# Performance work log

Measured on AMD Instinct MI355X. Metric: run time of the kernel, lower is better.

The kernel has to match this reference:

```python
import jax, jax.numpy as jnp
import numpy as np

B, Q, K, D = 32, 1024, 1024, 128

def setup_inputs() -> dict:
    key = jax.random.key(0)
    kq, kk, kv, kl = jax.random.split(key, 4)
    return {
        "queries": jax.random.normal(kq, (B, Q, D), dtype=jnp.float32),
        "keys": jax.random.normal(kk, (B, K, D), dtype=jnp.float32),
        "values": jax.random.normal(kv, (B, K, D), dtype=jnp.float32),
        "valid_length": jax.random.randint(kl, (B,), 1, K + 1),
    }

def reference(queries, keys, values, valid_length):
    d = queries.shape[-1]
    # scores: [B, Q, K]
    scores = jnp.einsum("bqd,bkd->bqk", queries, keys) / jnp.sqrt(jnp.float32(d))
    # length mask: position k is valid iff k < valid_length[b]
    mask = jnp.arange(keys.shape[1])[None, None, :] < valid_length[:, None, None]
    scores = jnp.where(mask, scores, jnp.float32(-1e9))
    attn = jax.nn.softmax(scores, axis=-1)
    # dropout module is identity in eval / p=0
    return jnp.einsum("bqk,bkv->bqv", attn, values)
```

## Files before the change

### kernel.cpp

```cpp
#include <hip/hip_runtime.h>
#include <hip/hip_bf16.h>
#include <stdint.h>

#define B_    32
#define QLEN  1024
#define KSEQ  1024
#define DIM   128
#define NKT   (KSEQ / 64)
#define SCALE 0.08838834764831845f

typedef __attribute__((ext_vector_type(8))) short  short8;
typedef __attribute__((ext_vector_type(4))) float  floatx4;
typedef unsigned int u32;

__device__ __forceinline__ u32 f2bf(float x) {
  union { float f; u32 u; } v; v.f = x;
  return (v.u + 0x7FFF + ((v.u >> 16) & 1)) >> 16;
}
__device__ __forceinline__ u32 pack2(float lo, float hi) {
  return f2bf(lo) | (f2bf(hi) << 16);
}

__device__ __forceinline__ void barrier_full() {
  asm volatile("s_waitcnt vmcnt(0) lgkmcnt(0)" ::: "memory");
  __syncthreads();
}

__global__ __launch_bounds__(256) void prep_kernel(const float* __restrict__ Kg,
                                                   const float* __restrict__ Vg,
                                                   const int* __restrict__ vlen,
                                                   uint4* __restrict__ Ksw,
                                                   uint4* __restrict__ Vsw) {
  const int kt = blockIdx.x, b = blockIdx.y, t = threadIdx.x;
  if (kt * 64 >= vlen[b]) return;
  if (blockIdx.z == 0) {
    const float* src = Kg + ((size_t)b * KSEQ + kt * 64) * DIM;
    uint4* dst = Ksw + ((size_t)b * NKT + kt) * 1024;
#pragma unroll
    for (int it = 0; it < 4; it++) {
      const int f = it * 256 + t, r = f >> 4, c = f & 15;
      floatx4 f0 = *(const floatx4*)(src + r * DIM + c * 8);
      floatx4 f1 = *(const floatx4*)(src + r * DIM + c * 8 + 4);
      uint4 o;
      o.x = pack2(f0[0], f0[1]); o.y = pack2(f0[2], f0[3]);
      o.z = pack2(f1[0], f1[1]); o.w = pack2(f1[2], f1[3]);
      dst[r * 16 + (c ^ (r & 15))] = o;
    }
  } else {
    const float* src = Vg + ((size_t)b * KSEQ + kt * 64) * DIM;
    uint4* dst = Vsw + ((size_t)b * NKT + kt) * 1024;
#pragma unroll
    for (int it = 0; it < 4; it++) {
      const int id = it * 256 + t, d = id & 127, kc = id >> 7;
      float v[8];
#pragma unroll
      for (int j = 0; j < 8; j++) v[j] = src[(size_t)(kc * 8 + j) * DIM + d];
      uint4 o;
      o.x = pack2(v[0], v[1]); o.y = pack2(v[2], v[3]);
      o.z = pack2(v[4], v[5]); o.w = pack2(v[6], v[7]);
      dst[d * 8 + (kc ^ (d & 7))] = o;
    }
  }
}

__global__ __launch_bounds__(256) void sched_kernel(const int* __restrict__ vlen,
                                                    int2* __restrict__ task) {
  __shared__ int sidx[32];
  const int t = threadIdx.x;
  if (t < 64) {
    const int b = t & 31;
    const int nt = (vlen[b] + 63) >> 6;
    int rank = 0;
#pragma unroll
    for (int j = 0; j < 32; j++) {
      const int ntj = __shfl(nt, j);
      rank += (ntj > nt) | ((ntj == nt) & (j < b));
    }
    if (t < 32) sidx[rank] = b;
  }
  __syncthreads();
  for (int l = t; l < 512; l += 256) {
    const int x = l & 7, j = l >> 3;
    int rank, q;
    if (j < 32) { rank = (j & 1) ? x + 8  : x;      q = j >> 1; }
    else        { rank = (j & 1) ? x + 16 : x + 24; q = (j - 32) >> 1; }
    task[l] = make_int2(sidx[rank], q << 6);
  }
}

typedef const __attribute__((address_space(1))) u32* as1p;
typedef __attribute__((address_space(3))) u32* as3p;
__device__ __forceinline__ void gl_lds16(const void* g, void* l) {
  __builtin_amdgcn_global_load_lds((as1p)g, (as3p)l, 16, 0, 0);
}

__global__ __launch_bounds__(256, 2) void attn_kernel(
    const float* __restrict__ Qg, const uint4* __restrict__ Ksw,
    const uint4* __restrict__ Vsw, const int* __restrict__ vlen,
    const int2* __restrict__ task, float* __restrict__ Og) {
  __shared__ __align__(16) short Kbuf[2][64 * 128];
  __shared__ __align__(16) short Vbuf[2][128 * 64];
  __shared__ __align__(16) short Pl[4][16][72];

  const int2 tq = task[blockIdx.x];
  const int b = tq.x, q0 = tq.y;
  const int t = threadIdx.x, wave = t >> 6, lane = t & 63;
  const int quad = lane >> 4, m = lane & 15;
  const int L  = vlen[b];
  const int nt = (L + 63) >> 6;

  const char* Kt = (const char*)(Ksw + (size_t)b * NKT * 1024);
  const char* Vt = (const char*)(Vsw + (size_t)b * NKT * 1024);

  short8 aq[4];
  {
    const float* qrow = Qg + ((size_t)b * QLEN + q0 + wave * 16 + m) * DIM;
#pragma unroll
    for (int c = 0; c < 4; c++) {
      floatx4 f0 = *(const floatx4*)(qrow + c * 32 + quad * 8);
      floatx4 f1 = *(const floatx4*)(qrow + c * 32 + quad * 8 + 4);
      short8 a;
      a[0] = (short)f2bf(f0[0]); a[1] = (short)f2bf(f0[1]);
      a[2] = (short)f2bf(f0[2]); a[3] = (short)f2bf(f0[3]);
      a[4] = (short)f2bf(f1[0]); a[5] = (short)f2bf(f1[1]);
      a[6] = (short)f2bf(f1[2]); a[7] = (short)f2bf(f1[3]);
      aq[c] = a;
    }
  }

  float lrow[4];
  floatx4 oacc[8];
#pragma unroll
  for (int r = 0; r < 4; r++) lrow[r] = 0.0f;
#pragma unroll
  for (int d = 0; d < 8; d++) oacc[d] = (floatx4){0.f, 0.f, 0.f, 0.f};

#define ISSUE_K(tk, bb)                                                        \
  {                                                                            \
    const char* g_ = Kt + (size_t)(tk) * 16384 + wave * 4096 + lane * 16;      \
    _Pragma("unroll") for (int i_ = 0; i_ < 4; i_++)                           \
        gl_lds16(g_ + i_ * 1024, (char*)Kbuf[bb] + wave * 4096 + i_ * 1024);   \
  }
#define ISSUE_V(tk, bb)                                                        \
  {                                                                            \
    const char* g_ = Vt + (size_t)(tk) * 16384 + wave * 4096 + lane * 16;      \
    _Pragma("unroll") for (int i_ = 0; i_ < 4; i_++)                           \
        gl_lds16(g_ + i_ * 1024, (char*)Vbuf[bb] + wave * 4096 + i_ * 1024);   \
  }

  ISSUE_K(0, 0);
  ISSUE_V(0, 0);

  for (int tk = 0; tk < nt; tk++) {
    const int k0 = tk * 64;
    barrier_full();
    if (tk + 1 < nt) {
      ISSUE_K(tk + 1, (tk + 1) & 1);
      ISSUE_V(tk + 1, (tk + 1) & 1);
    }
    const short* Kb_ = Kbuf[tk & 1];
    const short* Vb_ = Vbuf[tk & 1];

    floatx4 sa[4];
#pragma unroll
    for (int s = 0; s < 4; s++) sa[s] = (floatx4){0.f, 0.f, 0.f, 0.f};
#pragma unroll
    for (int s = 0; s < 4; s++) {
#pragma unroll
      for (int c = 0; c < 4; c++) {
        const short8 bk = *(const short8*)(Kb_ + (s * 16 + m) * 128 +
                                           (((c * 4 + quad) ^ m) & 15) * 8);
        sa[s] = __builtin_amdgcn_mfma_f32_16x16x32_bf16(aq[c], bk, sa[s], 0, 0, 0);
      }
    }

    float p[4][4];
    if (k0 + 64 <= L) {
#pragma unroll
      for (int s = 0; s < 4; s++)
#pragma unroll
        for (int r = 0; r < 4; r++)
          p[s][r] = __expf(fminf(sa[s][r] * SCALE, 30.0f));
    } else {
      const bool vv[4] = {(k0 + m) < L, (k0 + 16 + m) < L,
                          (k0 + 32 + m) < L, (k0 + 48 + m) < L};
#pragma unroll
      for (int s = 0; s < 4; s++)
#pragma unroll
        for (int r = 0; r < 4; r++)
          p[s][r] = vv[s] ? __expf(fminf(sa[s][r] * SCALE, 30.0f)) : 0.0f;
    }
#pragma unroll
    for (int r = 0; r < 4; r++)
      lrow[r] += (p[0][r] + p[1][r]) + (p[2][r] + p[3][r]);

#pragma unroll
    for (int s = 0; s < 4; s++) {
#pragma unroll
      for (int r = 0; r < 4; r++)
        Pl[wave][quad * 4 + r][s * 16 + m] = (short)f2bf(p[s][r]);
    }
    asm volatile("s_waitcnt lgkmcnt(0)" ::: "memory");
    const short8 pa0 = *(const short8*)&Pl[wave][m][quad * 8];
    const short8 pa1 = *(const short8*)&Pl[wave][m][32 + quad * 8];

#pragma unroll
    for (int d = 0; d < 8; d++) {
      const int row = d * 16 + m;
      const short8 bv0 = *(const short8*)(Vb_ + row * 64 + ((quad ^ (m & 7)) & 7) * 8);
      const short8 bv1 = *(const short8*)(Vb_ + row * 64 + (((quad + 4) ^ (m & 7)) & 7) * 8);
      oacc[d] = __builtin_amdgcn_mfma_f32_16x16x32_bf16(pa0, bv0, oacc[d], 0, 0, 0);
      oacc[d] = __builtin_amdgcn_mfma_f32_16x16x32_bf16(pa1, bv1, oacc[d], 0, 0, 0);
    }
  }

#pragma unroll
  for (int off = 1; off < 16; off <<= 1) {
#pragma unroll
    for (int r = 0; r < 4; r++) lrow[r] += __shfl_xor(lrow[r], off);
  }
  float inv[4];
#pragma unroll
  for (int r = 0; r < 4; r++) inv[r] = 1.0f / lrow[r];
  float* orow = Og + ((size_t)b * QLEN + q0 + wave * 16) * DIM;
#pragma unroll
  for (int d = 0; d < 8; d++) {
#pragma unroll
    for (int r = 0; r < 4; r++)
      orow[(size_t)(quad * 4 + r) * DIM + d * 16 + m] = oacc[d][r] * inv[r];
  }
#undef ISSUE_K
#undef ISSUE_V
}

extern "C" void kernel_launch(void* const* d_in, const int* in_sizes, int n_in,
                              void* d_out, int out_size, void* d_ws, size_t ws_size,
                              hipStream_t stream) {
  const float* Qg = (const float*)d_in[0];
  const float* Kg = (const float*)d_in[1];
  const float* Vg = (const float*)d_in[2];
  const int*  vln = (const int*)d_in[3];
  uint4* Ksw = (uint4*)d_ws;
  uint4* Vsw = (uint4*)((char*)d_ws + (size_t)B_ * NKT * 16384);
  int2*  Tsk = (int2*)((char*)d_ws + 2 * (size_t)B_ * NKT * 16384);

  sched_kernel<<<1, 256, 0, stream>>>(vln, Tsk);
  prep_kernel<<<dim3(NKT, B_, 2), 256, 0, stream>>>(Kg, Vg, vln, Ksw, Vsw);
  attn_kernel<<<dim3(512), 256, 0, stream>>>(Qg, Ksw, Vsw, vln, Tsk,
                                             (float*)d_out);
}
```

Before: 121.7 us.

## Fold scheduler into prep kernel, transpose V via LDS, raise MFMA priority

The task-table scheduler is merged into one block of the prep kernel, which removes a separate kernel launch. The V transpose-and-convert now uses coalesced float4 loads staged in LDS, then byte-permutes the packed bf16 pairs into the transposed swizzled layout, replacing strided scalar global loads. The attention kernel wraps its MFMA loops in s_setprio to favour matrix issue. The prep kernel gains a 16KB LDS buffer and an extra barrier, which may lower its occupancy.

```diff
diff --git a/kernel.cpp b/kernel.cpp
--- a/kernel.cpp
+++ b/kernel.cpp
@@ -30,61 +30,79 @@
                                                    const float* __restrict__ Vg,
                                                    const int* __restrict__ vlen,
                                                    uint4* __restrict__ Ksw,
-                                                   uint4* __restrict__ Vsw) {
+                                                   uint4* __restrict__ Vsw,
+                                                   int2* __restrict__ task) {
+  __shared__ __align__(16) u32 Vu[64 * 65];
+  __shared__ int sidx[32];
   const int kt = blockIdx.x, b = blockIdx.y, t = threadIdx.x;
-  if (kt * 64 >= vlen[b]) return;
-  if (blockIdx.z == 0) {
-    const float* src = Kg + ((size_t)b * KSEQ + kt * 64) * DIM;
-    uint4* dst = Ksw + ((size_t)b * NKT + kt) * 1024;
-#pragma unroll
-    for (int it = 0; it < 4; it++) {
-      const int f = it * 256 + t, r = f >> 4, c = f & 15;
-      floatx4 f0 = *(const floatx4*)(src + r * DIM + c * 8);
-      floatx4 f1 = *(const floatx4*)(src + r * DIM + c * 8 + 4);
-      uint4 o;
-      o.x = pack2(f0[0], f0[1]); o.y = pack2(f0[2], f0[3]);
-      o.z = pack2(f1[0], f1[1]); o.w = pack2(f1[2], f1[3]);
-      dst[r * 16 + (c ^ (r & 15))] = o;
-    }
-  } else {
-    const float* src = Vg + ((size_t)b * KSEQ + kt * 64) * DIM;
-    uint4* dst = Vsw + ((size_t)b * NKT + kt) * 1024;
-#pragma unroll
-    for (int it = 0; it < 4; it++) {
-      const int id = it * 256 + t, d = id & 127, kc = id >> 7;
-      float v[8];
-#pragma unroll
-      for (int j = 0; j < 8; j++) v[j] = src[(size_t)(kc * 8 + j) * DIM + d];
-      uint4 o;
-      o.x = pack2(v[0], v[1]); o.y = pack2(v[2], v[3]);
-      o.z = pack2(v[4], v[5]); o.w = pack2(v[6], v[7]);
-      dst[d * 8 + (kc ^ (d & 7))] = o;
-    }
-  }
-}
-
-__global__ __launch_bounds__(256) void sched_kernel(const int* __restrict__ vlen,
-                                                    int2* __restrict__ task) {
-  __shared__ int sidx[32];
-  const int t = threadIdx.x;
-  if (t < 64) {
-    const int b = t & 31;
-    const int nt = (vlen[b] + 63) >> 6;
+  const bool tableblk = (blockIdx.z == 0) && (kt == 0) && (b == 0);
+
+  if (tableblk && t < 64) {
+    const int bb = t & 31;
+    const int ntb = (vlen[bb] + 63) >> 6;
     int rank = 0;
 #pragma unroll
     for (int j = 0; j < 32; j++) {
-      const int ntj = __shfl(nt, j);
-      rank += (ntj > nt) | ((ntj == nt) & (j < b));
-    }
-    if (t < 32) sidx[rank] = b;
-  }
-  __syncthreads();
-  for (int l = t; l < 512; l += 256) {
-    const int x = l & 7, j = l >> 3;
-    int rank, q;
-    if (j < 32) { rank = (j & 1) ? x + 8  : x;      q = j >> 1; }
-    else        { rank = (j & 1) ? x + 16 : x + 24; q = (j - 32) >> 1; }
-    task[l] = make_int2(sidx[rank], q << 6);
+      const int ntj = __shfl(ntb, j);
+      rank += (ntj > ntb) | ((ntj == ntb) & (j < bb));
+    }
+    if (t < 32) sidx[rank] = bb;
+  }
+
+  if (kt * 64 < vlen[b]) {
+    if (blockIdx.z == 0) {
+      const float* src = Kg + ((size_t)b * KSEQ + kt * 64) * DIM;
+      uint4* dst = Ksw + ((size_t)b * NKT + kt) * 1024;
+#pragma unroll
+      for (int it = 0; it < 4; it++) {
+        const int f = it * 256 + t, r = f >> 4, c = f & 15;
+        floatx4 f0 = *(const floatx4*)(src + r * DIM + c * 8);
+        floatx4 f1 = *(const floatx4*)(src + r * DIM + c * 8 + 4);
+        uint4 o;
+        o.x = pack2(f0[0], f0[1]); o.y = pack2(f0[2], f0[3]);
+        o.z = pack2(f1[0], f1[1]); o.w = pack2(f1[2], f1[3]);
+        dst[r * 16 + (c ^ (r & 15))] = o;
+      }
+    } else {
+      const float* src = Vg + ((size_t)b * KSEQ + kt * 64) * DIM;
+#pragma unroll
+      for (int it = 0; it < 8; it++) {
+        const int k = it * 8 + (t >> 5), c = t & 31;
+        const floatx4 f = *(const floatx4*)(src + (size_t)k * DIM + c * 4);
+        const int s = (k >> 3) & 4;
+        Vu[k * 65 + ((2 * c) ^ s)]     = pack2(f[0], f[1]);
+        Vu[k * 65 + ((2 * c + 1) ^ s)] = pack2(f[2], f[3]);
+      }
+      __syncthreads();
+      uint4* dst = Vsw + ((size_t)b * NKT + kt) * 1024;
+#pragma unroll
+      for (int it = 0; it < 4; it++) {
+        const int id = it * 256 + t;
+        const int kc = id & 7, d = (id >> 3) & 127;
+        const int col = (d >> 1) ^ (kc & 4);
+        u32 r[8];
+#pragma unroll
+        for (int j = 0; j < 8; j++) r[j] = Vu[(kc * 8 + j) * 65 + col];
+        const u32 sel = (d & 1) ? 0x07060302u : 0x05040100u;
+        uint4 o;
+        o.x = __builtin_amdgcn_perm(r[1], r[0], sel);
+        o.y = __builtin_amdgcn_perm(r[3], r[2], sel);
+        o.z = __builtin_amdgcn_perm(r[5], r[4], sel);
+        o.w = __builtin_amdgcn_perm(r[7], r[6], sel);
+        dst[d * 8 + (kc ^ (d & 7))] = o;
+      }
+    }
+  }
+
+  if (tableblk) {
+    __syncthreads();
+    for (int l = t; l < 512; l += 256) {
+      const int x = l & 7, j = l >> 3;
+      int rank, q;
+      if (j < 32) { rank = (j & 1) ? x + 8  : x;      q = j >> 1; }
+      else        { rank = (j & 1) ? x + 16 : x + 24; q = (j - 32) >> 1; }
+      task[l] = make_int2(sidx[rank], q << 6);
+    }
   }
 }
 
@@ -164,6 +182,7 @@
     floatx4 sa[4];
 #pragma unroll
     for (int s = 0; s < 4; s++) sa[s] = (floatx4){0.f, 0.f, 0.f, 0.f};
+    __builtin_amdgcn_s_setprio(1);
 #pragma unroll
     for (int s = 0; s < 4; s++) {
 #pragma unroll
@@ -173,6 +192,7 @@
         sa[s] = __builtin_amdgcn_mfma_f32_16x16x32_bf16(aq[c], bk, sa[s], 0, 0, 0);
       }
     }
+    __builtin_amdgcn_s_setprio(0);
 
     float p[4][4];
     if (k0 + 64 <= L) {
@@ -204,6 +224,7 @@
     const short8 pa0 = *(const short8*)&Pl[wave][m][quad * 8];
     const short8 pa1 = *(const short8*)&Pl[wave][m][32 + quad * 8];
 
+    __builtin_amdgcn_s_setprio(1);
 #pragma unroll
     for (int d = 0; d < 8; d++) {
       const int row = d * 16 + m;
@@ -212,6 +233,7 @@
       oacc[d] = __builtin_amdgcn_mfma_f32_16x16x32_bf16(pa0, bv0, oacc[d], 0, 0, 0);
       oacc[d] = __builtin_amdgcn_mfma_f32_16x16x32_bf16(pa1, bv1, oacc[d], 0, 0, 0);
     }
+    __builtin_amdgcn_s_setprio(0);
   }
 
 #pragma unroll
@@ -244,8 +266,7 @@
   uint4* Vsw = (uint4*)((char*)d_ws + (size_t)B_ * NKT * 16384);
   int2*  Tsk = (int2*)((char*)d_ws + 2 * (size_t)B_ * NKT * 16384);
 
-  sched_kernel<<<1, 256, 0, stream>>>(vln, Tsk);
-  prep_kernel<<<dim3(NKT, B_, 2), 256, 0, stream>>>(Kg, Vg, vln, Ksw, Vsw);
+  prep_kernel<<<dim3(NKT, B_, 2), 256, 0, stream>>>(Kg, Vg, vln, Ksw, Vsw, Tsk);
   attn_kernel<<<dim3(512), 256, 0, stream>>>(Qg, Ksw, Vsw, vln, Tsk,
                                              (float*)d_out);
 }
```

Result: faster. 118.5 us (-2.7%).
